# Kernel optimization log

Hardware: AMD Instinct MI355X
Metric: run time of the kernel (lower is better)

The kernel has to match this reference:

```python
import jax, jax.numpy as jnp
import numpy as np

N = 50000          # nodes
E = 3_200_000      # edges (radius-graph topology, avg degree ~64)
C = 10             # node channels
ED = 4             # edge_dim: [dist, dx, dy, food_flag]
H = 16             # message hidden dim
RADIUS = 0.05
ACC_SCALE = 0.005
MAX_VEL = 0.02
EDGES_TO_STAY_ALIVE = 3
CONSUMPTION_EDGES_REQUIRED = 3
NOISE_SCALE = 0.004


def setup_inputs() -> dict:
    key = jax.random.key(0)
    ks = jax.random.split(key, 10)
    pos = jax.random.uniform(ks[0], (N, 2), minval=-1.0, maxval=1.0)
    vel = jax.random.uniform(ks[1], (N, 2), minval=-MAX_VEL, maxval=MAX_VEL)
    # column 4: 1.0 = living cell, 0.0 = food node
    is_cell = (jax.random.uniform(ks[2], (N,)) > 0.2).astype(jnp.float32)
    hidden = jax.random.normal(ks[3], (N, C - 5)) * 0.1
    x = jnp.concatenate([pos, vel, is_cell[:, None], hidden], axis=1)  # [N,10]
    src = jax.random.randint(ks[4], (E,), 0, N)
    dst = jax.random.randint(ks[5], (E,), 0, N)
    noise = jax.random.uniform(ks[6], (N, 2))  # uniform [0,1), mapped to [-1,1) inside
    W_edge = jax.random.normal(ks[7], (ED, H)) * 0.3
    W_src = jax.random.normal(ks[8], (C, H)) * 0.3
    b1 = jnp.zeros((H,), jnp.float32)
    W_out = jax.random.normal(ks[9], (H, 4)) * 0.3
    b2 = jnp.zeros((4,), jnp.float32)
    return dict(x=x, src=src, dst=dst, noise=noise, W_edge=W_edge,
                W_src=W_src, b1=b1, W_out=W_out, b2=b2)


def reference(x, src, dst, noise, W_edge, W_src, b1, W_out, b2):
    pos = x[:, :2]
    vel = x[:, 2:4]
    cell = x[:, 4]
    c_mask = (cell == 1.0).astype(x.dtype)          # [N]

    # ---- edge attributes of the (dynamic) radius graph ----
    d = pos[src] - pos[dst]                          # [E,2] gather
    dist = jnp.sqrt(jnp.sum(d * d, axis=1) + 1e-12)  # [E]
    food_flag = cell[src]                            # 0 for food-source edges
    edge_attr = jnp.concatenate([dist[:, None], d, food_flag[:, None]], axis=1)  # [E,4]

    # ---- message passing: per-edge MLP + scatter-sum + node readout ----
    m = jax.nn.relu(edge_attr @ W_edge + x[src] @ W_src + b1)     # [E,H]
    agg = jax.ops.segment_sum(m, dst, num_segments=N)             # [N,H]
    h = jnp.tanh(agg @ W_out + b2) * c_mask[:, None]              # [N,4], masked as in update_graph

    # ---- velocity / position update ----
    acc = h[:, :2] * ACC_SCALE
    new_vel = jnp.clip(vel + acc, -MAX_VEL, MAX_VEL)
    new_pos = pos + new_vel                                       # wrap_around = False
    vel_noisy = new_vel + (noise * 2.0 - 1.0) * NOISE_SCALE * c_mask[:, None]
    new_x = jnp.concatenate(
        [new_pos, vel_noisy, cell[:, None], h[:, 2:], x[:, 7:]], axis=1)  # [N,10]

    # ---- costs / stats ----
    eps = 1e-6
    border_mask = (jnp.abs(new_pos) > 1.0).astype(x.dtype)        # [N,2]
    border_cost = jnp.sum(jnp.log(jnp.abs(new_pos) + eps) * border_mask)
    food_edge = (food_flag == 0.0)
    visible_food = food_edge.sum()
    mean_food_dist = jnp.sum(dist * food_edge.astype(x.dtype))

    # ---- node removal masks (jit-safe: return keep mask instead of slicing) ----
    deg = jax.ops.segment_sum(jnp.ones_like(dist), dst, num_segments=N)
    dead = (cell == 1.0) & (deg < EDGES_TO_STAY_ALIVE)
    consume_e = (dist < RADIUS) & (cell[src] == 1.0) & (cell[dst] == 0.0)
    cdeg = jax.ops.segment_sum(consume_e.astype(x.dtype), dst, num_segments=N)
    consumed = (cell == 0.0) & (cdeg >= CONSUMPTION_EDGES_REQUIRED)
    keep_mask = ~(dead | consumed)

    velocity_bonus = jnp.mean(jnp.abs(new_vel), axis=0)           # [2]
    dead_cost = dead.sum()
    food_reward = consumed.sum()
    return (new_x, keep_mask, velocity_bonus, border_cost, food_reward,
            dead_cost, visible_food, mean_food_dist)
```

## Files before the change

### kernel.cpp

```cpp
#include <hip/hip_runtime.h>
#include <math.h>

#define NN 50000
#define NE 3200000

#define NT    98
#define TSZ   512
#define CAP   34816
#define SCB   1250
#define EPB   2560
#define EPT   10

static constexpr float ACC_SCALE   = 0.005f;
static constexpr float MAX_VEL     = 0.02f;
static constexpr float NOISE_SCALE = 0.004f;
static constexpr float RADIUS      = 0.05f;

#define OUT_KEEP   500000
#define OUT_SCAL   550000

#define WS_NI    0
#define WS_S2    200704
#define WS_GCUR  1003520
#define WS_BK    1005120
#define WS_PACC  4417088

__global__ __launch_bounds__(256) void k1_prep(
    const float* __restrict__ x,
    const float* __restrict__ W_edge,
    const float* __restrict__ W_src,
    const float* __restrict__ b1,
    float4* __restrict__ nodeinfo,
    float4* __restrict__ s2,
    int* __restrict__ gcur,
    float* __restrict__ out_scalars)
{
    int n = blockIdx.x * 256 + threadIdx.x;
    if (blockIdx.x == 0) {
        if (threadIdx.x < 7) out_scalars[threadIdx.x] = 0.0f;
        for (int i = threadIdx.x; i < NT * 16; i += 256)
            gcur[i] = (i & 15) ? 0 : (i >> 4) * CAP;
    }
    if (n >= NN) return;

    float xr[10];
#pragma unroll
    for (int c = 0; c < 10; ++c) xr[c] = x[n * 10 + c];
    float cell = xr[4];

    nodeinfo[n] = make_float4(xr[0], xr[1], cell, 0.0f);

    float v[16];
#pragma unroll
    for (int j = 0; j < 16; ++j) {
        float a = fmaf(cell, W_edge[48 + j], b1[j]);
#pragma unroll
        for (int c = 0; c < 10; ++c) a = fmaf(xr[c], W_src[c * 16 + j], a);
        v[j] = a;
    }
#pragma unroll
    for (int q = 0; q < 4; ++q)
        s2[(size_t)n * 4 + q] = make_float4(v[q*4], v[q*4+1], v[q*4+2], v[q*4+3]);
}

__global__ __launch_bounds__(256) void k_scatter(
    const int* __restrict__ src,
    const int* __restrict__ dst,
    int* __restrict__ gcur,
    unsigned* __restrict__ bucket)
{
    __shared__ unsigned stage[EPB];
    __shared__ int hist[NT], binstart[NT], lcur[NT], gbase[NT];
    __shared__ int scanbuf[128];

    int tid = threadIdx.x;
    for (int i = tid; i < NT; i += 256) { hist[i] = 0; lcur[i] = 0; }
    __syncthreads();

    int e0 = blockIdx.x * EPB;

    int d[EPT];
#pragma unroll
    for (int j = 0; j < EPT; ++j) d[j] = dst[e0 + j * 256 + tid];
#pragma unroll
    for (int j = 0; j < EPT; ++j) atomicAdd(&hist[d[j] >> 9], 1);
    __syncthreads();

    if (tid < 128) scanbuf[tid] = (tid < NT) ? hist[tid] : 0;
    __syncthreads();
    for (int off = 1; off < 128; off <<= 1) {
        int v = 0;
        if (tid < 128 && tid >= off) v = scanbuf[tid - off];
        __syncthreads();
        if (tid < 128) scanbuf[tid] += v;
        __syncthreads();
    }
    if (tid < NT) {
        int bs = scanbuf[tid] - hist[tid];
        binstart[tid] = bs;
        gbase[tid] = atomicAdd(&gcur[tid * 16], hist[tid]) - bs;
    }
    __syncthreads();

    int sreg[EPT];
#pragma unroll
    for (int j = 0; j < EPT; ++j) sreg[j] = src[e0 + j * 256 + tid];
#pragma unroll
    for (int j = 0; j < EPT; ++j) {
        int t = d[j] >> 9;
        int pos = binstart[t] + atomicAdd(&lcur[t], 1);
        stage[pos] = (unsigned)sreg[j] | ((unsigned)(d[j] & 511) << 16)
                   | ((unsigned)t << 25);
    }
    __syncthreads();

#pragma unroll
    for (int j = 0; j < EPT; ++j) {
        int i = j * 256 + tid;
        unsigned e = stage[i];
        int b = e >> 25;
        int g = gbase[b] + i;
        if (g < (b + 1) * CAP) bucket[g] = e;
    }
}

__global__ __launch_bounds__(256, 6) void k_agg(
    const float* __restrict__ W_edge,
    const float* __restrict__ W_out,
    const float4* __restrict__ nodeinfo,
    const float* __restrict__ s2,
    const int* __restrict__ gcur,
    const unsigned* __restrict__ bucket,
    float4* __restrict__ pacc,
    int* __restrict__ pdeg,
    float* __restrict__ out_scalars,
    int lg)
{
    __shared__ float sAcc[TSZ][5];
    __shared__ int   sDeg[TSZ];
    __shared__ float sPX[TSZ], sPY[TSZ], sCL[TSZ];
    __shared__ float sRed[4][2];

    int t   = blockIdx.x >> lg;
    int sl  = blockIdx.x & ((1 << lg) - 1);
    int nsl = 1 << lg;
    int tid = threadIdx.x;

    for (int j = tid; j < TSZ; j += 256) {
        int g = t * TSZ + j;
        float4 ni = (g < NN) ? nodeinfo[g] : make_float4(9e9f, 9e9f, -1.f, 0.f);
        sPX[j] = ni.x; sPY[j] = ni.y; sCL[j] = ni.z;
        sAcc[j][0] = 0.f; sAcc[j][1] = 0.f; sAcc[j][2] = 0.f; sAcc[j][3] = 0.f;
        sDeg[j] = 0;
    }

    float w0[16], w1[16], w2[16], woa[16], wob[16], woc[16], wod[16];
#pragma unroll
    for (int k = 0; k < 16; ++k) {
        w0[k] = W_edge[k];
        w1[k] = W_edge[16 + k];
        w2[k] = W_edge[32 + k];
        woa[k] = W_out[k * 4 + 0];
        wob[k] = W_out[k * 4 + 1];
        woc[k] = W_out[k * 4 + 2];
        wod[k] = W_out[k * 4 + 3];
    }
    __syncthreads();

    int cnt = gcur[t * 16] - t * CAP;
    if (cnt > CAP) cnt = CAP;
    int cs = (cnt + nsl - 1) / nsl;
    int i0 = sl * cs;
    int i1 = min(i0 + cs, cnt);

    const unsigned* bk = bucket + (size_t)t * CAP;
    float vis = 0.f, fd = 0.f;

    int i = i0 + tid;
    int ic = min(i, i1 - 1); if (ic < 0) ic = 0;
    unsigned eA = bk[ic];
    int sA = eA & 0xFFFF;
    float4 niA = nodeinfo[sA];
    const float4* rA = (const float4*)(s2 + (size_t)sA * 16);
    float4 a0 = rA[0], a1 = rA[1], a2 = rA[2], a3 = rA[3];

    for (; i < i1; i += 256) {
        int icn = min(i + 256, i1 - 1);
        unsigned eB = bk[icn];
        int sB = eB & 0xFFFF;
        float4 niB = nodeinfo[sB];
        const float4* rB = (const float4*)(s2 + (size_t)sB * 16);
        float4 b0 = rB[0], b1v = rB[1], b2v = rB[2], b3v = rB[3];

        int dl = (eA >> 16) & 0x1FF;
        float dx = niA.x - sPX[dl];
        float dy = niA.y - sPY[dl];
        float ctl = sCL[dl];
        float dist = sqrtf(fmaf(dx, dx, fmaf(dy, dy, 1e-12f)));

        bool food0 = (niA.z == 0.0f);
        vis += food0 ? 1.f : 0.f;
        fd  += food0 ? dist : 0.f;

        bool consume = (dist < RADIUS) && (niA.z == 1.0f) && (ctl == 0.0f);
        atomicAdd(&sDeg[dl], consume ? 65537 : 1);

        float sv[16] = { a0.x, a0.y, a0.z, a0.w, a1.x, a1.y, a1.z, a1.w,
                         a2.x, a2.y, a2.z, a2.w, a3.x, a3.y, a3.z, a3.w };
        float v0 = 0.f, v1 = 0.f, v2 = 0.f, v3 = 0.f;
#pragma unroll
        for (int k = 0; k < 16; ++k) {
            float m = fmaf(dist, w0[k], fmaf(dx, w1[k], fmaf(dy, w2[k], sv[k])));
            m = fmaxf(m, 0.0f);
            v0 = fmaf(m, woa[k], v0);
            v1 = fmaf(m, wob[k], v1);
            v2 = fmaf(m, woc[k], v2);
            v3 = fmaf(m, wod[k], v3);
        }
        atomicAdd(&sAcc[dl][0], v0);
        atomicAdd(&sAcc[dl][1], v1);
        atomicAdd(&sAcc[dl][2], v2);
        atomicAdd(&sAcc[dl][3], v3);

        eA = eB; niA = niB; a0 = b0; a1 = b1v; a2 = b2v; a3 = b3v;
    }
    __syncthreads();

    for (int j = tid; j < TSZ; j += 256) {
        int o = sl * (NT * TSZ) + t * TSZ + j;
        pacc[o] = make_float4(sAcc[j][0], sAcc[j][1], sAcc[j][2], sAcc[j][3]);
        pdeg[o] = sDeg[j];
    }

#pragma unroll
    for (int off = 32; off > 0; off >>= 1) {
        vis += __shfl_down(vis, off);
        fd  += __shfl_down(fd,  off);
    }
    int lane = tid & 63, wv = tid >> 6;
    if (lane == 0) { sRed[wv][0] = vis; sRed[wv][1] = fd; }
    __syncthreads();
    if (tid == 0) {
        float a = 0.f, b = 0.f;
#pragma unroll
        for (int wq = 0; wq < 4; ++wq) { a += sRed[wq][0]; b += sRed[wq][1]; }
        atomicAdd(&out_scalars[5], a);
        atomicAdd(&out_scalars[6], b);
    }
}

__global__ __launch_bounds__(256) void k_final(
    const float* __restrict__ x,
    const float* __restrict__ noise,
    const float* __restrict__ b2,
    const float4* __restrict__ pacc,
    const int* __restrict__ pdeg,
    float* __restrict__ out,
    float* __restrict__ out_scalars,
    int nsl)
{
    __shared__ float sRed[4][5];
    int tid  = threadIdx.x;
    int n    = blockIdx.x * 128 + (tid >> 1);
    int half = tid & 1;

    float a0 = 0.f, a1 = 0.f, a2 = 0.f, a3 = 0.f;
    int dp = 0;
    if (n < NN) {
        for (int sl = half; sl < nsl; sl += 2) {
            float4 q = pacc[(size_t)sl * (NT * TSZ) + n];
            a0 += q.x; a1 += q.y; a2 += q.z; a3 += q.w;
            dp += pdeg[(size_t)sl * (NT * TSZ) + n];
        }
    }
    a0 += __shfl_xor(a0, 1);
    a1 += __shfl_xor(a1, 1);
    a2 += __shfl_xor(a2, 1);
    a3 += __shfl_xor(a3, 1);
    dp += __shfl_xor(dp, 1);

    float avx = 0.f, avy = 0.f, bc = 0.f, deadf = 0.f, consf = 0.f;
    if (n < NN && half == 0) {
        float cell = x[n * 10 + 4];
        float cm = (cell == 1.0f) ? 1.0f : 0.0f;
        float h0 = tanhf(a0 + b2[0]) * cm;
        float h1 = tanhf(a1 + b2[1]) * cm;
        float h2 = tanhf(a2 + b2[2]) * cm;
        float h3 = tanhf(a3 + b2[3]) * cm;

        float px = x[n * 10 + 0], py = x[n * 10 + 1];
        float vx = x[n * 10 + 2], vy = x[n * 10 + 3];

        float nvx = fminf(fmaxf(fmaf(h0, ACC_SCALE, vx), -MAX_VEL), MAX_VEL);
        float nvy = fminf(fmaxf(fmaf(h1, ACC_SCALE, vy), -MAX_VEL), MAX_VEL);
        float npx = px + nvx;
        float npy = py + nvy;

        float vnx = nvx + (noise[n * 2 + 0] * 2.0f - 1.0f) * NOISE_SCALE * cm;
        float vny = nvy + (noise[n * 2 + 1] * 2.0f - 1.0f) * NOISE_SCALE * cm;

        float* row = out + (size_t)n * 10;
        row[0] = npx;  row[1] = npy;
        row[2] = vnx;  row[3] = vny;
        row[4] = cell; row[5] = h2;  row[6] = h3;
        row[7] = x[n * 10 + 7];
        row[8] = x[n * 10 + 8];
        row[9] = x[n * 10 + 9];

        float apx = fabsf(npx), apy = fabsf(npy);
        if (apx > 1.0f) bc += logf(apx + 1e-6f);
        if (apy > 1.0f) bc += logf(apy + 1e-6f);

        int deg  = dp & 0xFFFF;
        int cdeg = dp >> 16;
        bool dead = (cell == 1.0f) && (deg < 3);
        bool cons = (cell == 0.0f) && (cdeg >= 3);
        out[OUT_KEEP + n] = (dead || cons) ? 0.0f : 1.0f;
        deadf = dead ? 1.0f : 0.0f;
        consf = cons ? 1.0f : 0.0f;
        avx = fabsf(nvx) * (1.0f / NN);
        avy = fabsf(nvy) * (1.0f / NN);
    }

    float r[5] = { avx, avy, bc, consf, deadf };
#pragma unroll
    for (int q = 0; q < 5; ++q) {
#pragma unroll
        for (int off = 32; off > 0; off >>= 1)
            r[q] += __shfl_down(r[q], off);
    }
    int lane = tid & 63, wv = tid >> 6;
    if (lane == 0) {
#pragma unroll
        for (int q = 0; q < 5; ++q) sRed[wv][q] = r[q];
    }
    __syncthreads();
    if (tid == 0) {
#pragma unroll
        for (int q = 0; q < 5; ++q) {
            float acc = sRed[0][q] + sRed[1][q] + sRed[2][q] + sRed[3][q];
            atomicAdd(&out_scalars[q], acc);
        }
    }
}

extern "C" void kernel_launch(void* const* d_in, const int* in_sizes, int n_in,
                              void* d_out, int out_size, void* d_ws, size_t ws_size,
                              hipStream_t stream) {
    const float* x      = (const float*)d_in[0];
    const int*   src    = (const int*)  d_in[1];
    const int*   dst    = (const int*)  d_in[2];
    const float* noise  = (const float*)d_in[3];
    const float* W_edge = (const float*)d_in[4];
    const float* W_src  = (const float*)d_in[5];
    const float* b1     = (const float*)d_in[6];
    const float* W_out  = (const float*)d_in[7];
    const float* b2     = (const float*)d_in[8];

    size_t need16 = ((size_t)WS_PACC + 16ull * NT * TSZ * 5) * 4;
    int lg  = (ws_size >= need16) ? 4 : 3;
    int nsl = 1 << lg;

    float* ws = (float*)d_ws;
    float4*   nodeinfo = (float4*)(ws + WS_NI);
    float*    s2       = ws + WS_S2;
    int*      gcur     = (int*)(ws + WS_GCUR);
    unsigned* bucket   = (unsigned*)(ws + WS_BK);
    float4*   pacc     = (float4*)(ws + WS_PACC);
    int*      pdeg     = (int*)(ws + WS_PACC + (size_t)nsl * NT * TSZ * 4);

    float* out         = (float*)d_out;
    float* out_scalars = out + OUT_SCAL;

    k1_prep<<<196, 256, 0, stream>>>(
        x, W_edge, W_src, b1, nodeinfo, (float4*)s2, gcur, out_scalars);

    k_scatter<<<SCB, 256, 0, stream>>>(src, dst, gcur, bucket);

    k_agg<<<NT * nsl, 256, 0, stream>>>(
        W_edge, W_out, nodeinfo, s2, gcur, bucket, pacc, pdeg,
        out_scalars, lg);

    k_final<<<392, 256, 0, stream>>>(
        x, noise, b2, pacc, pdeg, out, out_scalars, nsl);
}
```

Before: 243.7 us.

## Pack per-node source record with fp16 features and simplify aggregation gather loop

Stores each node's position, cell flag and 16 precomputed source features as one 48-byte record, with the features in fp16, so each edge gathers three float4s instead of one nodeinfo float4 plus four feature float4s. The aggregation loop drops manual prefetching in favor of unroll-by-4 with nontemporal bucket loads. It also fixes the slice count at 8, doubles edges per scatter block, staggers the per-block global cursor atomics and uses nontemporal bucket stores. fp16 rounding of the source features reduces accuracy, and removing the explicit prefetch may expose more gather latency.

```diff
diff --git a/kernel.cpp b/kernel.cpp
--- a/kernel.cpp
+++ b/kernel.cpp
@@ -1,4 +1,5 @@
 #include <hip/hip_runtime.h>
+#include <hip/hip_fp16.h>
 #include <math.h>
 
 #define NN 50000
@@ -7,9 +8,10 @@
 #define NT    98
 #define TSZ   512
 #define CAP   34816
-#define SCB   1250
-#define EPB   2560
-#define EPT   10
+#define SCB   625
+#define EPB   5120
+#define EPT   20
+#define NSL   8
 
 static constexpr float ACC_SCALE   = 0.005f;
 static constexpr float MAX_VEL     = 0.02f;
@@ -20,10 +22,11 @@
 #define OUT_SCAL   550000
 
 #define WS_NI    0
-#define WS_S2    200704
-#define WS_GCUR  1003520
-#define WS_BK    1005120
-#define WS_PACC  4417088
+#define WS_SREC  200704
+#define WS_GCUR  802816
+#define WS_BK    804416
+#define WS_PACC  4216384
+#define WS_PDEG  5822016
 
 __global__ __launch_bounds__(256) void k1_prep(
     const float* __restrict__ x,
@@ -31,7 +34,7 @@
     const float* __restrict__ W_src,
     const float* __restrict__ b1,
     float4* __restrict__ nodeinfo,
-    float4* __restrict__ s2,
+    float4* __restrict__ srec,
     int* __restrict__ gcur,
     float* __restrict__ out_scalars)
 {
@@ -58,9 +61,20 @@
         for (int c = 0; c < 10; ++c) a = fmaf(xr[c], W_src[c * 16 + j], a);
         v[j] = a;
     }
-#pragma unroll
-    for (int q = 0; q < 4; ++q)
-        s2[(size_t)n * 4 + q] = make_float4(v[q*4], v[q*4+1], v[q*4+2], v[q*4+3]);
+
+    float4 r1, r2;
+    r1.x = __builtin_bit_cast(float, __floats2half2_rn(v[0],  v[1]));
+    r1.y = __builtin_bit_cast(float, __floats2half2_rn(v[2],  v[3]));
+    r1.z = __builtin_bit_cast(float, __floats2half2_rn(v[4],  v[5]));
+    r1.w = __builtin_bit_cast(float, __floats2half2_rn(v[6],  v[7]));
+    r2.x = __builtin_bit_cast(float, __floats2half2_rn(v[8],  v[9]));
+    r2.y = __builtin_bit_cast(float, __floats2half2_rn(v[10], v[11]));
+    r2.z = __builtin_bit_cast(float, __floats2half2_rn(v[12], v[13]));
+    r2.w = __builtin_bit_cast(float, __floats2half2_rn(v[14], v[15]));
+
+    srec[(size_t)n * 3 + 0] = make_float4(xr[0], xr[1], cell, 0.0f);
+    srec[(size_t)n * 3 + 1] = r1;
+    srec[(size_t)n * 3 + 2] = r2;
 }
 
 __global__ __launch_bounds__(256) void k_scatter(
@@ -96,9 +110,10 @@
         __syncthreads();
     }
     if (tid < NT) {
-        int bs = scanbuf[tid] - hist[tid];
-        binstart[tid] = bs;
-        gbase[tid] = atomicAdd(&gcur[tid * 16], hist[tid]) - bs;
+        int tt = (tid + blockIdx.x) % NT;
+        int bs = scanbuf[tt] - hist[tt];
+        binstart[tt] = bs;
+        gbase[tt] = atomicAdd(&gcur[tt * 16], hist[tt]) - bs;
     }
     __syncthreads();
 
@@ -120,30 +135,28 @@
         unsigned e = stage[i];
         int b = e >> 25;
         int g = gbase[b] + i;
-        if (g < (b + 1) * CAP) bucket[g] = e;
-    }
-}
-
-__global__ __launch_bounds__(256, 6) void k_agg(
+        if (g < (b + 1) * CAP) __builtin_nontemporal_store(e, &bucket[g]);
+    }
+}
+
+__global__ __launch_bounds__(256) void k_agg(
     const float* __restrict__ W_edge,
     const float* __restrict__ W_out,
     const float4* __restrict__ nodeinfo,
-    const float* __restrict__ s2,
+    const float4* __restrict__ srec,
     const int* __restrict__ gcur,
     const unsigned* __restrict__ bucket,
     float4* __restrict__ pacc,
     int* __restrict__ pdeg,
-    float* __restrict__ out_scalars,
-    int lg)
+    float* __restrict__ out_scalars)
 {
     __shared__ float sAcc[TSZ][5];
     __shared__ int   sDeg[TSZ];
     __shared__ float sPX[TSZ], sPY[TSZ], sCL[TSZ];
     __shared__ float sRed[4][2];
 
-    int t   = blockIdx.x >> lg;
-    int sl  = blockIdx.x & ((1 << lg) - 1);
-    int nsl = 1 << lg;
+    int t   = blockIdx.x >> 3;
+    int sl  = blockIdx.x & 7;
     int tid = threadIdx.x;
 
     for (int j = tid; j < TSZ; j += 256) {
@@ -169,44 +182,48 @@
 
     int cnt = gcur[t * 16] - t * CAP;
     if (cnt > CAP) cnt = CAP;
-    int cs = (cnt + nsl - 1) / nsl;
+    int cs = (cnt + NSL - 1) / NSL;
     int i0 = sl * cs;
     int i1 = min(i0 + cs, cnt);
 
     const unsigned* bk = bucket + (size_t)t * CAP;
     float vis = 0.f, fd = 0.f;
 
-    int i = i0 + tid;
-    int ic = min(i, i1 - 1); if (ic < 0) ic = 0;
-    unsigned eA = bk[ic];
-    int sA = eA & 0xFFFF;
-    float4 niA = nodeinfo[sA];
-    const float4* rA = (const float4*)(s2 + (size_t)sA * 16);
-    float4 a0 = rA[0], a1 = rA[1], a2 = rA[2], a3 = rA[3];
-
-    for (; i < i1; i += 256) {
-        int icn = min(i + 256, i1 - 1);
-        unsigned eB = bk[icn];
-        int sB = eB & 0xFFFF;
-        float4 niB = nodeinfo[sB];
-        const float4* rB = (const float4*)(s2 + (size_t)sB * 16);
-        float4 b0 = rB[0], b1v = rB[1], b2v = rB[2], b3v = rB[3];
-
-        int dl = (eA >> 16) & 0x1FF;
-        float dx = niA.x - sPX[dl];
-        float dy = niA.y - sPY[dl];
-        float ctl = sCL[dl];
+#pragma unroll 4
+    for (int i = i0 + tid; i < i1; i += 256) {
+        unsigned e = __builtin_nontemporal_load(&bk[i]);
+        int s  = e & 0xFFFF;
+        int dl = (e >> 16) & 0x1FF;
+
+        const float4* r = srec + (size_t)s * 3;
+        float4 r0 = r[0];
+        float4 r1 = r[1];
+        float4 r2 = r[2];
+
+        float dx = r0.x - sPX[dl];
+        float dy = r0.y - sPY[dl];
         float dist = sqrtf(fmaf(dx, dx, fmaf(dy, dy, 1e-12f)));
 
-        bool food0 = (niA.z == 0.0f);
+        bool food0 = (r0.z == 0.0f);
         vis += food0 ? 1.f : 0.f;
         fd  += food0 ? dist : 0.f;
 
-        bool consume = (dist < RADIUS) && (niA.z == 1.0f) && (ctl == 0.0f);
+        bool consume = (dist < RADIUS) && (r0.z == 1.0f) && (sCL[dl] == 0.0f);
         atomicAdd(&sDeg[dl], consume ? 65537 : 1);
 
-        float sv[16] = { a0.x, a0.y, a0.z, a0.w, a1.x, a1.y, a1.z, a1.w,
-                         a2.x, a2.y, a2.z, a2.w, a3.x, a3.y, a3.z, a3.w };
+        float sv[16];
+        {
+            float2 f;
+            f = __half22float2(__builtin_bit_cast(__half2, r1.x)); sv[0]=f.x;  sv[1]=f.y;
+            f = __half22float2(__builtin_bit_cast(__half2, r1.y)); sv[2]=f.x;  sv[3]=f.y;
+            f = __half22float2(__builtin_bit_cast(__half2, r1.z)); sv[4]=f.x;  sv[5]=f.y;
+            f = __half22float2(__builtin_bit_cast(__half2, r1.w)); sv[6]=f.x;  sv[7]=f.y;
+            f = __half22float2(__builtin_bit_cast(__half2, r2.x)); sv[8]=f.x;  sv[9]=f.y;
+            f = __half22float2(__builtin_bit_cast(__half2, r2.y)); sv[10]=f.x; sv[11]=f.y;
+            f = __half22float2(__builtin_bit_cast(__half2, r2.z)); sv[12]=f.x; sv[13]=f.y;
+            f = __half22float2(__builtin_bit_cast(__half2, r2.w)); sv[14]=f.x; sv[15]=f.y;
+        }
+
         float v0 = 0.f, v1 = 0.f, v2 = 0.f, v3 = 0.f;
 #pragma unroll
         for (int k = 0; k < 16; ++k) {
@@ -221,8 +238,6 @@
         atomicAdd(&sAcc[dl][1], v1);
         atomicAdd(&sAcc[dl][2], v2);
         atomicAdd(&sAcc[dl][3], v3);
-
-        eA = eB; niA = niB; a0 = b0; a1 = b1v; a2 = b2v; a3 = b3v;
     }
     __syncthreads();
 
@@ -256,8 +271,7 @@
     const float4* __restrict__ pacc,
     const int* __restrict__ pdeg,
     float* __restrict__ out,
-    float* __restrict__ out_scalars,
-    int nsl)
+    float* __restrict__ out_scalars)
 {
     __shared__ float sRed[4][5];
     int tid  = threadIdx.x;
@@ -267,10 +281,12 @@
     float a0 = 0.f, a1 = 0.f, a2 = 0.f, a3 = 0.f;
     int dp = 0;
     if (n < NN) {
-        for (int sl = half; sl < nsl; sl += 2) {
-            float4 q = pacc[(size_t)sl * (NT * TSZ) + n];
+#pragma unroll
+        for (int sl = 0; sl < NSL / 2; ++sl) {
+            int o = (2 * sl + half) * (NT * TSZ) + n;
+            float4 q = pacc[o];
             a0 += q.x; a1 += q.y; a2 += q.z; a3 += q.w;
-            dp += pdeg[(size_t)sl * (NT * TSZ) + n];
+            dp += pdeg[o];
         }
     }
     a0 += __shfl_xor(a0, 1);
@@ -357,30 +373,25 @@
     const float* W_out  = (const float*)d_in[7];
     const float* b2     = (const float*)d_in[8];
 
-    size_t need16 = ((size_t)WS_PACC + 16ull * NT * TSZ * 5) * 4;
-    int lg  = (ws_size >= need16) ? 4 : 3;
-    int nsl = 1 << lg;
-
     float* ws = (float*)d_ws;
     float4*   nodeinfo = (float4*)(ws + WS_NI);
-    float*    s2       = ws + WS_S2;
+    float4*   srec     = (float4*)(ws + WS_SREC);
     int*      gcur     = (int*)(ws + WS_GCUR);
     unsigned* bucket   = (unsigned*)(ws + WS_BK);
     float4*   pacc     = (float4*)(ws + WS_PACC);
-    int*      pdeg     = (int*)(ws + WS_PACC + (size_t)nsl * NT * TSZ * 4);
+    int*      pdeg     = (int*)(ws + WS_PDEG);
 
     float* out         = (float*)d_out;
     float* out_scalars = out + OUT_SCAL;
 
     k1_prep<<<196, 256, 0, stream>>>(
-        x, W_edge, W_src, b1, nodeinfo, (float4*)s2, gcur, out_scalars);
+        x, W_edge, W_src, b1, nodeinfo, srec, gcur, out_scalars);
 
     k_scatter<<<SCB, 256, 0, stream>>>(src, dst, gcur, bucket);
 
-    k_agg<<<NT * nsl, 256, 0, stream>>>(
-        W_edge, W_out, nodeinfo, s2, gcur, bucket, pacc, pdeg,
-        out_scalars, lg);
+    k_agg<<<NT * NSL, 256, 0, stream>>>(
+        W_edge, W_out, nodeinfo, srec, gcur, bucket, pacc, pdeg, out_scalars);
 
     k_final<<<392, 256, 0, stream>>>(
-        x, noise, b2, pacc, pdeg, out, out_scalars, nsl);
-}
+        x, noise, b2, pacc, pdeg, out, out_scalars);
+}
```

After: 229.2 us. -5.9%, faster.
